# Kernel optimization log

Measured on AMD Instinct MI355X. Metric: run time of the kernel, lower is better.

## Reference

```python
import jax, jax.numpy as jnp
from jax import lax
import numpy as np

B = 128          # batch size
S = 207          # input spatial size implied by outputSpatialSize=[8,8]
N_PTS = 256000
NEG = -1e30      # -inf stand-in for masked max-pooling
# BNReLU channel counts in execution order: 8 resnet blocks x (bn1, bn2), final resnet BN(32), last BN(64)
SIZES = [8,8,8,8,8,16,16,16,16,24,24,24,24,32,32,32,32,64]
OFF = np.cumsum([0] + SIZES)

WSHAPES = dict(conv0=(3,3,1,8),
               c1a=(3,3,8,8), c1b=(3,3,8,8), c2a=(3,3,8,8), c2b=(3,3,8,8),
               c3a=(3,3,8,16), c3b=(3,3,16,16), c3r=(3,3,8,16),
               c4a=(3,3,16,16), c4b=(3,3,16,16),
               c5a=(3,3,16,24), c5b=(3,3,24,24), c5r=(3,3,16,24),
               c6a=(3,3,24,24), c6b=(3,3,24,24),
               c7a=(3,3,24,32), c7b=(3,3,32,32), c7r=(3,3,24,32),
               c8a=(3,3,32,32), c8b=(3,3,32,32),
               conv_last=(5,5,32,64))

def _conv(x, w, stride, padding):
    return lax.conv_general_dilated(x, w, (stride, stride), padding,
                                    dimension_numbers=('NHWC', 'HWIO', 'NHWC'))

def _pool_max(x, win, stride, init):
    return lax.reduce_window(x, init, lax.max, (1, win, win, 1), (1, stride, stride, 1), 'VALID')

def _bnrelu(x, m, g, b):
    # eval-mode BN folded to affine, applied on active sites only (inactive stay exactly 0)
    return m * jax.nn.relu(x * g + b)

def _subconv(x, w, m):
    # submanifold conv == dense conv on zero-filled grid, output restricted to active sites
    return _conv(x, w, 1, 'SAME') * m

def _strided(x, w, m, win, stride):
    # scn.Convolution: output site active iff any active input in its receptive field
    m2 = _pool_max(m, win, stride, 0.0)
    return _conv(x, w, stride, 'VALID') * m2, m2

def _block(x, m, g1, b1, w1, g2, b2, w2, wres, stride):
    # pre-activation basic block from scn.SparseResNet
    h = _bnrelu(x, m, g1, b1)
    if stride == 1:
        h, m2 = _subconv(h, w1, m), m
    else:
        h, m2 = _strided(h, w1, m, 3, 2)
    h = _subconv(_bnrelu(h, m2, g2, b2), w2, m2)
    r = x if wres is None else _strided(x, wres, m, 3, 2)[0]
    return h + r, m2

def _forward(locations, batch_idx, features, bn_gamma, bn_beta, W):
    idx = (batch_idx, locations[:, 0], locations[:, 1], jnp.zeros_like(batch_idx))
    x = jnp.zeros((B, S, S, 1), jnp.float32).at[idx].add(features[:, 0])  # InputLayer (sum dups)
    m = jnp.zeros((B, S, S, 1), jnp.float32).at[idx].set(1.0)             # active-site mask
    g = [bn_gamma[OFF[i]:OFF[i+1]] for i in range(len(SIZES))]
    b = [bn_beta[OFF[i]:OFF[i+1]] for i in range(len(SIZES))]
    x = _subconv(x, W['conv0'], m)                              # 1->8 @ 207x207
    # MaxPooling(pool 3, stride 2) over active sites only
    m2 = _pool_max(m, 3, 2, 0.0)
    x = jnp.where(m2 > 0, _pool_max(jnp.where(m > 0, x, NEG), 3, 2, NEG), 0.0)
    m = m2                                                      # @ 103x103
    blocks = [('c1a', 'c1b', None, 1), ('c2a', 'c2b', None, 1),
              ('c3a', 'c3b', 'c3r', 2), ('c4a', 'c4b', None, 1),
              ('c5a', 'c5b', 'c5r', 2), ('c6a', 'c6b', None, 1),
              ('c7a', 'c7b', 'c7r', 2), ('c8a', 'c8b', None, 1)]
    for i, (k1, k2, kr, st) in enumerate(blocks):
        x, m = _block(x, m, g[2*i], b[2*i], W[k1], g[2*i+1], b[2*i+1], W[k2],
                      None if kr is None else W[kr], st)        # 103->51->25->12
    x = _bnrelu(x, m, g[16], b[16])                             # final resnet BNReLU(32)
    x, m = _strided(x, W['conv_last'], m, 5, 1)                 # 32->64, 12x12 -> 8x8
    x = _bnrelu(x, m, g[17], b[17])
    flat = x.transpose(0, 3, 1, 2).reshape(B, -1)               # SparseToDense + flatten (NCHW order)
    return (flat @ W['w_lin'].T).reshape(B, -1, 1)              # [B, 100, 1]

def setup_inputs():
    key = jax.random.key(0)
    ks = iter(jax.random.split(key, 64))
    inp = {
        'locations': jax.random.randint(next(ks), (N_PTS, 2), 0, S, dtype=jnp.int32),
        'batch_idx': jax.random.randint(next(ks), (N_PTS,), 0, B, dtype=jnp.int32),
        'features': jax.random.normal(next(ks), (N_PTS, 1), jnp.float32),
        'bn_gamma': 1.0 + 0.1 * jax.random.normal(next(ks), (int(OFF[-1]),), jnp.float32),
        'bn_beta': 0.1 * jax.random.normal(next(ks), (int(OFF[-1]),), jnp.float32),
    }
    for name, shp in WSHAPES.items():
        fan_in = int(np.prod(shp[:-1]))
        inp[name] = jax.random.normal(next(ks), shp, jnp.float32) * (2.0 / fan_in) ** 0.5
    inp['w_lin'] = jax.random.normal(next(ks), (100, 64 * 8 * 8), jnp.float32) * (1.0 / 4096.0) ** 0.5
    return inp

def reference(locations, batch_idx, features, bn_gamma, bn_beta, conv0,
              c1a, c1b, c2a, c2b, c3a, c3b, c3r, c4a, c4b, c5a, c5b, c5r,
              c6a, c6b, c7a, c7b, c7r, c8a, c8b, conv_last, w_lin):
    W = dict(conv0=conv0, c1a=c1a, c1b=c1b, c2a=c2a, c2b=c2b, c3a=c3a, c3b=c3b, c3r=c3r,
             c4a=c4a, c4b=c4b, c5a=c5a, c5b=c5b, c5r=c5r, c6a=c6a, c6b=c6b,
             c7a=c7a, c7b=c7b, c7r=c7r, c8a=c8a, c8b=c8b, conv_last=conv_last, w_lin=w_lin)
    return _forward(locations, batch_idx, features, bn_gamma, bn_beta, W)
```

## Files before the change

### kernel.cpp

```cpp
#include <hip/hip_runtime.h>

#define S 207
#define BATCH 128
#define NPTS 256000

static const int OFFS[19] = {0,8,16,24,32,40,56,72,88,104,128,152,176,200,232,264,296,328,392};

__global__ void zero2_kernel(float4* __restrict__ a, float4* __restrict__ b, int n4) {
    int i = blockIdx.x * blockDim.x + threadIdx.x;
    if (i < n4) { a[i] = make_float4(0,0,0,0); b[i] = make_float4(0,0,0,0); }
}

__global__ void zero_kernel(float* __restrict__ p, int n) {
    int i = blockIdx.x * blockDim.x + threadIdx.x;
    if (i < n) p[i] = 0.0f;
}

__global__ void scatter_kernel(const int* __restrict__ loc, const int* __restrict__ bidx,
                               const float* __restrict__ feat,
                               float* __restrict__ xs, float* __restrict__ ms) {
    int t = blockIdx.x * blockDim.x + threadIdx.x;
    if (t >= NPTS) return;
    int b = bidx[t];
    int r = loc[2 * t];
    int c = loc[2 * t + 1];
    int idx = (b * S + r) * S + c;
    atomicAdd(&xs[idx], feat[t]);
    ms[idx] = 1.0f;
}

__global__ __launch_bounds__(256) void conv0_pool_kernel(
    const float* __restrict__ xs, const float* __restrict__ ms,
    const float* __restrict__ w,
    float* __restrict__ x1, float* __restrict__ m1) {
    const int Hout = 103;
    int opix = blockIdx.x * 256 + threadIdx.x;
    int total = BATCH * Hout * Hout;
    if (opix >= total) return;
    int wo = opix % Hout;
    int t = opix / Hout;
    int ho = t % Hout;
    int b  = t / Hout;

    float mv[3][3];
    float mwin = 0.0f;
    #pragma unroll
    for (int pi = 0; pi < 3; ++pi)
        #pragma unroll
        for (int pj = 0; pj < 3; ++pj) {
            float m = ms[(b * S + 2 * ho + pi) * S + 2 * wo + pj];
            mv[pi][pj] = m;
            mwin = fmaxf(mwin, m);
        }
    float* xp = x1 + (size_t)opix * 8;
    if (mwin <= 0.0f) {
        *(float4*)xp = make_float4(0,0,0,0);
        *(float4*)(xp + 4) = make_float4(0,0,0,0);
        m1[opix] = 0.0f;
        return;
    }
    float p[5][5];
    #pragma unroll
    for (int r = 0; r < 5; ++r) {
        int ii = 2 * ho - 1 + r;
        #pragma unroll
        for (int c = 0; c < 5; ++c) {
            int jj = 2 * wo - 1 + c;
            bool ok = ((unsigned)ii < (unsigned)S) && ((unsigned)jj < (unsigned)S);
            p[r][c] = ok ? xs[(b * S + ii) * S + jj] : 0.0f;
        }
    }
    float best[8];
    #pragma unroll
    for (int co = 0; co < 8; ++co) best[co] = -1e30f;
    #pragma unroll
    for (int pi = 0; pi < 3; ++pi)
        #pragma unroll
        for (int pj = 0; pj < 3; ++pj) {
            if (mv[pi][pj] > 0.0f) {
                float acc[8];
                #pragma unroll
                for (int co = 0; co < 8; ++co) acc[co] = 0.0f;
                #pragma unroll
                for (int kh = 0; kh < 3; ++kh)
                    #pragma unroll
                    for (int kw = 0; kw < 3; ++kw) {
                        float x = p[pi + kh][pj + kw];
                        #pragma unroll
                        for (int co = 0; co < 8; ++co)
                            acc[co] = fmaf(x, w[(kh * 3 + kw) * 8 + co], acc[co]);
                    }
                #pragma unroll
                for (int co = 0; co < 8; ++co) best[co] = fmaxf(best[co], acc[co]);
            }
        }
    *(float4*)xp = make_float4(best[0], best[1], best[2], best[3]);
    *(float4*)(xp + 4) = make_float4(best[4], best[5], best[6], best[7]);
    m1[opix] = 1.0f;
}

template <int C, int TILE, int NTX>
__global__ __launch_bounds__(256) void resblock_kernel(
    const float* __restrict__ in, const float* __restrict__ mask,
    const float* __restrict__ w1, const float* __restrict__ w2,
    const float* __restrict__ g1, const float* __restrict__ bb1,
    const float* __restrict__ g2, const float* __restrict__ bb2,
    float* __restrict__ out, int H) {
    constexpr int XT = TILE + 4, HT = TILE + 2;
    constexpr int XA = XT * XT, HA = HT * HT;
    __shared__ float xs[C][XA];
    __shared__ float h1[C][HA];
    __shared__ float msh[XA];

    int tid = threadIdx.x;
    int bid = blockIdx.x;
    int b = bid / (NTX * NTX);
    int t = bid % (NTX * NTX);
    int r0 = (t / NTX) * TILE, c0 = (t % NTX) * TILE;

    float gr[C], br[C];
    #pragma unroll
    for (int c = 0; c < C; ++c) { gr[c] = g1[c]; br[c] = bb1[c]; }

    for (int i = tid; i < XA; i += 256) {
        int py = i / XT, px = i % XT;
        int gy = r0 - 2 + py, gx = c0 - 2 + px;
        bool ok = (unsigned)gy < (unsigned)H && (unsigned)gx < (unsigned)H;
        float m = 0.0f;
        if (ok) m = mask[(size_t)(b * H + gy) * H + gx];
        msh[i] = m;
        if (m > 0.0f) {
            const float* ip = in + ((size_t)(b * H + gy) * H + gx) * C;
            #pragma unroll
            for (int c = 0; c < C; ++c)
                xs[c][i] = m * fmaxf(fmaf(ip[c], gr[c], br[c]), 0.0f);
        } else {
            #pragma unroll
            for (int c = 0; c < C; ++c) xs[c][i] = 0.0f;
        }
    }
    #pragma unroll
    for (int c = 0; c < C; ++c) { gr[c] = g2[c]; br[c] = bb2[c]; }
    __syncthreads();

    for (int pos = tid; pos < HA; pos += 256) {
        int py = pos / HT, px = pos % HT;
        float mc = msh[(py + 1) * XT + px + 1];
        float acc[C];
        #pragma unroll
        for (int co = 0; co < C; ++co) acc[co] = 0.0f;
        if (mc > 0.0f) {
            #pragma unroll
            for (int kh = 0; kh < 3; ++kh)
                #pragma unroll
                for (int kw = 0; kw < 3; ++kw) {
                    int pix = (py + kh) * XT + px + kw;
                    const float* wp = w1 + (kh * 3 + kw) * C * C;
                    #pragma unroll
                    for (int ci = 0; ci < C; ++ci) {
                        float xv = xs[ci][pix];
                        #pragma unroll
                        for (int co = 0; co < C; ++co)
                            acc[co] = fmaf(xv, wp[ci * C + co], acc[co]);
                    }
                }
        }
        #pragma unroll
        for (int co = 0; co < C; ++co)
            h1[co][pos] = mc * fmaxf(fmaf(acc[co] * mc, gr[co], br[co]), 0.0f);
    }
    __syncthreads();

    {
        int ty = tid / TILE, tx = tid % TILE;
        int gy = r0 + ty, gx = c0 + tx;
        if (gy < H && gx < H) {
            float mo = msh[(ty + 2) * XT + tx + 2];
            float acc[C];
            #pragma unroll
            for (int co = 0; co < C; ++co) acc[co] = 0.0f;
            if (mo > 0.0f) {
                #pragma unroll
                for (int kh = 0; kh < 3; ++kh)
                    #pragma unroll
                    for (int kw = 0; kw < 3; ++kw) {
                        int pix = (ty + kh) * HT + tx + kw;
                        const float* wp = w2 + (kh * 3 + kw) * C * C;
                        #pragma unroll
                        for (int ci = 0; ci < C; ++ci) {
                            float xv = h1[ci][pix];
                            #pragma unroll
                            for (int co = 0; co < C; ++co)
                                acc[co] = fmaf(xv, wp[ci * C + co], acc[co]);
                        }
                    }
            }
            const float* rp = in + ((size_t)(b * H + gy) * H + gx) * C;
            float* op = out + ((size_t)(b * H + gy) * H + gx) * C;
            #pragma unroll
            for (int j = 0; j < C; j += 4) {
                float4 r4 = *(const float4*)(rp + j);
                float4 o4;
                o4.x = fmaf(acc[j],     mo, r4.x);
                o4.y = fmaf(acc[j + 1], mo, r4.y);
                o4.z = fmaf(acc[j + 2], mo, r4.z);
                o4.w = fmaf(acc[j + 3], mo, r4.w);
                *(float4*)(op + j) = o4;
            }
        }
    }
}

template <int K, int CIN, int COUT, int COT, bool BN, bool RES>
__global__ __launch_bounds__(256) void fconv_kernel(
    const float* __restrict__ in, const float* __restrict__ w,
    const float* __restrict__ g, const float* __restrict__ bbn,
    const float* __restrict__ mIn, const float* __restrict__ mOut,
    const float* __restrict__ res, float* __restrict__ out,
    int Hin, int Hout, int stride, int pad) {
    const int Win = Hin, Wout = Hout;
    int npix = BATCH * Hout * Wout;
    int opix = blockIdx.x * 256 + threadIdx.x;
    if (opix >= npix) return;
    int co0 = blockIdx.y * COT;
    int wo = opix % Wout;
    int t = opix / Wout;
    int ho = t % Hout;
    int b  = t / Hout;

    float mo = mOut[opix];
    float* op = out + (size_t)opix * COUT + co0;
    if (mo <= 0.0f) {
        #pragma unroll
        for (int j = 0; j < COT; j += 4) {
            float4 r4 = RES ? *(const float4*)(res + (size_t)opix * COUT + co0 + j)
                            : make_float4(0,0,0,0);
            *(float4*)(op + j) = r4;
        }
        return;
    }
    float acc[COT];
    #pragma unroll
    for (int j = 0; j < COT; ++j) acc[j] = 0.0f;

    #pragma unroll
    for (int kh = 0; kh < K; ++kh) {
        int ih = ho * stride + kh - pad;
        if ((unsigned)ih >= (unsigned)Hin) continue;
        #pragma unroll
        for (int kw = 0; kw < K; ++kw) {
            int iw = wo * stride + kw - pad;
            if ((unsigned)iw >= (unsigned)Win) continue;
            int ipix = (b * Hin + ih) * Win + iw;
            float mi = 1.0f;
            if (BN) { mi = mIn[ipix]; if (mi <= 0.0f) continue; }
            const float* ip = in + (size_t)ipix * CIN;
            const float* wp = w + (kh * K + kw) * CIN * COUT + co0;
            #pragma unroll
            for (int ci = 0; ci < CIN; ci += 4) {
                float4 xv = *(const float4*)(ip + ci);
                if (BN) {
                    xv.x = mi * fmaxf(fmaf(xv.x, g[ci],     bbn[ci]),     0.0f);
                    xv.y = mi * fmaxf(fmaf(xv.y, g[ci + 1], bbn[ci + 1]), 0.0f);
                    xv.z = mi * fmaxf(fmaf(xv.z, g[ci + 2], bbn[ci + 2]), 0.0f);
                    xv.w = mi * fmaxf(fmaf(xv.w, g[ci + 3], bbn[ci + 3]), 0.0f);
                }
                #pragma unroll
                for (int j = 0; j < COT; ++j) {
                    acc[j] = fmaf(xv.x, wp[(ci    ) * COUT + j], acc[j]);
                    acc[j] = fmaf(xv.y, wp[(ci + 1) * COUT + j], acc[j]);
                    acc[j] = fmaf(xv.z, wp[(ci + 2) * COUT + j], acc[j]);
                    acc[j] = fmaf(xv.w, wp[(ci + 3) * COUT + j], acc[j]);
                }
            }
        }
    }
    #pragma unroll
    for (int j = 0; j < COT; j += 4) {
        float4 o4;
        o4.x = acc[j] * mo; o4.y = acc[j+1] * mo; o4.z = acc[j+2] * mo; o4.w = acc[j+3] * mo;
        if (RES) {
            float4 r4 = *(const float4*)(res + (size_t)opix * COUT + co0 + j);
            o4.x += r4.x; o4.y += r4.y; o4.z += r4.z; o4.w += r4.w;
        }
        *(float4*)(op + j) = o4;
    }
}

template <int CIN, int COUT, int COT>
__global__ __launch_bounds__(256) void strided_ra_kernel(
    const float* __restrict__ in,
    const float* __restrict__ wR, const float* __restrict__ wA,
    const float* __restrict__ g, const float* __restrict__ bbn,
    const float* __restrict__ mIn, float* __restrict__ mOutBuf,
    float* __restrict__ outR, float* __restrict__ outA,
    int Hin, int Hout) {
    constexpr int NG = COUT / COT;
    int npix = BATCH * Hout * Hout;
    int opix = blockIdx.x * 256 + threadIdx.x;
    if (opix >= npix) return;
    int path = blockIdx.y / NG;
    int co0  = (blockIdx.y % NG) * COT;
    int wo = opix % Hout;
    int t = opix / Hout;
    int ho = t % Hout;
    int b  = t / Hout;

    const float* wsel = path ? wA : wR;
    float acc[COT];
    #pragma unroll
    for (int j = 0; j < COT; ++j) acc[j] = 0.0f;
    float m2 = 0.0f;

    #pragma unroll
    for (int kh = 0; kh < 3; ++kh) {
        int ih = 2 * ho + kh;
        #pragma unroll
        for (int kw = 0; kw < 3; ++kw) {
            int iw = 2 * wo + kw;
            int ipix = (b * Hin + ih) * Hin + iw;
            float mi = mIn[ipix];
            if (mi <= 0.0f) continue;
            m2 = fmaxf(m2, mi);
            const float* ip = in + (size_t)ipix * CIN;
            const float* wp = wsel + (kh * 3 + kw) * CIN * COUT + co0;
            #pragma unroll
            for (int ci = 0; ci < CIN; ci += 4) {
                float4 xv = *(const float4*)(ip + ci);
                if (path) {
                    xv.x = mi * fmaxf(fmaf(xv.x, g[ci],     bbn[ci]),     0.0f);
                    xv.y = mi * fmaxf(fmaf(xv.y, g[ci + 1], bbn[ci + 1]), 0.0f);
                    xv.z = mi * fmaxf(fmaf(xv.z, g[ci + 2], bbn[ci + 2]), 0.0f);
                    xv.w = mi * fmaxf(fmaf(xv.w, g[ci + 3], bbn[ci + 3]), 0.0f);
                }
                #pragma unroll
                for (int j = 0; j < COT; ++j) {
                    acc[j] = fmaf(xv.x, wp[(ci    ) * COUT + j], acc[j]);
                    acc[j] = fmaf(xv.y, wp[(ci + 1) * COUT + j], acc[j]);
                    acc[j] = fmaf(xv.z, wp[(ci + 2) * COUT + j], acc[j]);
                    acc[j] = fmaf(xv.w, wp[(ci + 3) * COUT + j], acc[j]);
                }
            }
        }
    }
    if (blockIdx.y == 0) mOutBuf[opix] = m2;
    float* op = (path ? outA : outR) + (size_t)opix * COUT + co0;
    #pragma unroll
    for (int j = 0; j < COT; j += 4) {
        float4 o4;
        o4.x = acc[j] * m2; o4.y = acc[j+1] * m2; o4.z = acc[j+2] * m2; o4.w = acc[j+3] * m2;
        *(float4*)(op + j) = o4;
    }
}

__global__ void pool_kernel(const float* __restrict__ in, float* __restrict__ out,
                            int Hin, int Win, int Hout, int Wout, int win, int stride) {
    int tid = blockIdx.x * blockDim.x + threadIdx.x;
    int total = BATCH * Hout * Wout;
    if (tid >= total) return;
    int wo = tid % Wout;
    int p = tid / Wout;
    int ho = p % Hout;
    int b  = p / Hout;
    float mx = 0.0f;
    for (int i = 0; i < win; ++i)
        for (int j = 0; j < win; ++j)
            mx = fmaxf(mx, in[(b * Hin + ho * stride + i) * Win + wo * stride + j]);
    out[tid] = mx;
}

__global__ __launch_bounds__(256) void bn_tr_kernel(
    const float* __restrict__ x, const float* __restrict__ m,
    const float* __restrict__ g, const float* __restrict__ bb,
    float* __restrict__ xt) {
    int tid = blockIdx.x * 256 + threadIdx.x;
    if (tid >= BATCH * 4096) return;
    int c = tid & 63, hw = (tid >> 6) & 63, b = tid >> 12;
    float v = m[b * 64 + hw] * fmaxf(fmaf(x[tid], g[c], bb[c]), 0.0f);
    xt[((size_t)b << 12) + c * 64 + hw] = v;
}

__global__ __launch_bounds__(256) void linear_gemm_kernel(
    const float* __restrict__ xt, const float* __restrict__ wl,
    float* __restrict__ out) {
    int o = blockIdx.x;
    int half = threadIdx.x >> 7;
    int b = threadIdx.x & 127;
    int k0 = blockIdx.y * 512 + half * 256;
    const float* xp = xt + ((size_t)b << 12) + k0;
    const float* wp = wl + o * 4096 + k0;
    float acc = 0.0f;
    #pragma unroll 16
    for (int k = 0; k < 256; k += 4) {
        float4 xv = *(const float4*)(xp + k);
        float4 wv = *(const float4*)(wp + k);
        acc = fmaf(xv.x, wv.x, acc); acc = fmaf(xv.y, wv.y, acc);
        acc = fmaf(xv.z, wv.z, acc); acc = fmaf(xv.w, wv.w, acc);
    }
    atomicAdd(&out[b * 100 + o], acc);
}

template <int K, int CIN, int COUT, int COT, bool BN, bool RES>
static inline void fconv(hipStream_t s, const float* in, const float* w,
                         const float* g, const float* bbn,
                         const float* mIn, const float* mOut, const float* res,
                         float* out, int Hin, int Hout, int stride, int pad) {
    int npix = BATCH * Hout * Hout;
    dim3 grid((npix + 255) / 256, COUT / COT);
    fconv_kernel<K, CIN, COUT, COT, BN, RES><<<grid, 256, 0, s>>>(
        in, w, g, bbn, mIn, mOut, res, out, Hin, Hout, stride, pad);
}

template <int CIN, int COUT, int COT>
static inline void strided_ra(hipStream_t s, const float* in, const float* wR, const float* wA,
                              const float* g, const float* bbn, const float* mIn,
                              float* mOutBuf, float* outR, float* outA, int Hin, int Hout) {
    int npix = BATCH * Hout * Hout;
    dim3 grid((npix + 255) / 256, 2 * (COUT / COT));
    strided_ra_kernel<CIN, COUT, COT><<<grid, 256, 0, s>>>(
        in, wR, wA, g, bbn, mIn, mOutBuf, outR, outA, Hin, Hout);
}

extern "C" void kernel_launch(void* const* d_in, const int* in_sizes, int n_in,
                              void* d_out, int out_size, void* d_ws, size_t ws_size,
                              hipStream_t stream) {
    const int*   loc   = (const int*)d_in[0];
    const int*   bidx  = (const int*)d_in[1];
    const float* feat  = (const float*)d_in[2];
    const float* gamma = (const float*)d_in[3];
    const float* beta  = (const float*)d_in[4];
    const float* Wconv0 = (const float*)d_in[5];
    const float* Wc1a = (const float*)d_in[6];
    const float* Wc1b = (const float*)d_in[7];
    const float* Wc2a = (const float*)d_in[8];
    const float* Wc2b = (const float*)d_in[9];
    const float* Wc3a = (const float*)d_in[10];
    const float* Wc3b = (const float*)d_in[11];
    const float* Wc3r = (const float*)d_in[12];
    const float* Wc4a = (const float*)d_in[13];
    const float* Wc4b = (const float*)d_in[14];
    const float* Wc5a = (const float*)d_in[15];
    const float* Wc5b = (const float*)d_in[16];
    const float* Wc5r = (const float*)d_in[17];
    const float* Wc6a = (const float*)d_in[18];
    const float* Wc6b = (const float*)d_in[19];
    const float* Wc7a = (const float*)d_in[20];
    const float* Wc7b = (const float*)d_in[21];
    const float* Wc7r = (const float*)d_in[22];
    const float* Wc8a = (const float*)d_in[23];
    const float* Wc8b = (const float*)d_in[24];
    const float* Wlast = (const float*)d_in[25];
    const float* wlin  = (const float*)d_in[26];

    const size_t SZB = (size_t)BATCH * 103 * 103 * 8;
    const size_t SZM = (size_t)BATCH * 103 * 103;
    float* b0 = (float*)d_ws;
    float* b1 = b0 + SZB;
    float* b2 = b1 + SZB;
    float* m0 = b2 + SZB;
    float* m1 = m0 + SZM;

    const float* G[18];
    const float* Bt[18];
    for (int i = 0; i < 18; ++i) { G[i] = gamma + OFFS[i]; Bt[i] = beta + OFFS[i]; }

    {
        int n = BATCH * S * S;
        zero2_kernel<<<(n / 4 + 255) / 256, 256, 0, stream>>>((float4*)b1, (float4*)b2, n / 4);
        scatter_kernel<<<(NPTS + 255) / 256, 256, 0, stream>>>(loc, bidx, feat, b1, b2);
        int total = BATCH * 103 * 103;
        conv0_pool_kernel<<<(total + 255) / 256, 256, 0, stream>>>(b1, b2, Wconv0, b0, m0);
    }

    resblock_kernel<8, 16, 7><<<dim3(7 * 7 * BATCH), 256, 0, stream>>>(
        b0, m0, Wc1a, Wc1b, G[0], Bt[0], G[1], Bt[1], b1, 103);
    resblock_kernel<8, 16, 7><<<dim3(7 * 7 * BATCH), 256, 0, stream>>>(
        b1, m0, Wc2a, Wc2b, G[2], Bt[2], G[3], Bt[3], b2, 103);
    strided_ra<8, 16, 16>(stream, b2, Wc3r, Wc3a, G[4], Bt[4], m0, m1, b0, b1, 103, 51);
    fconv<3, 16, 16, 8, true, true >(stream, b1, Wc3b, G[5], Bt[5], m1, m1, b0, b2, 51, 51, 1, 1);
    fconv<3, 16, 16, 8, true, false>(stream, b2, Wc4a, G[6], Bt[6], m1, m1, nullptr, b0, 51, 51, 1, 1);
    fconv<3, 16, 16, 8, true, true >(stream, b0, Wc4b, G[7], Bt[7], m1, m1, b2,      b1, 51, 51, 1, 1);
    strided_ra<16, 24, 24>(stream, b1, Wc5r, Wc5a, G[8], Bt[8], m1, m0, b0, b2, 51, 25);
    fconv<3, 24, 24, 8, true, true >(stream, b2, Wc5b, G[9], Bt[9], m0, m0, b0, b1, 25, 25, 1, 1);
    fconv<3, 24, 24, 8, true, false>(stream, b1, Wc6a, G[10], Bt[10], m0, m0, nullptr, b0, 25, 25, 1, 1);
    fconv<3, 24, 24, 8, true, true >(stream, b0, Wc6b, G[11], Bt[11], m0, m0, b1,      b2, 25, 25, 1, 1);
    strided_ra<24, 32, 8>(stream, b2, Wc7r, Wc7a, G[12], Bt[12], m0, m1, b0, b1, 25, 12);
    fconv<3, 32, 32, 4, true, true >(stream, b1, Wc7b, G[13], Bt[13], m1, m1, b0, b2, 12, 12, 1, 1);
    fconv<3, 32, 32, 4, true, false>(stream, b2, Wc8a, G[14], Bt[14], m1, m1, nullptr, b0, 12, 12, 1, 1);
    fconv<3, 32, 32, 4, true, true >(stream, b0, Wc8b, G[15], Bt[15], m1, m1, b2,      b1, 12, 12, 1, 1);
    pool_kernel<<<(BATCH * 64 + 255) / 256, 256, 0, stream>>>(m1, m0, 12, 12, 8, 8, 5, 1);
    fconv<5, 32, 64, 4, true, false>(stream, b1, Wlast, G[16], Bt[16], m1, m0, nullptr, b0, 12, 8, 1, 0);
    bn_tr_kernel<<<(BATCH * 4096 + 255) / 256, 256, 0, stream>>>(b0, m0, G[17], Bt[17], b2);
    zero_kernel<<<(BATCH * 100 + 255) / 256, 256, 0, stream>>>((float*)d_out, BATCH * 100);
    linear_gemm_kernel<<<dim3(100, 8), 256, 0, stream>>>(b2, wlin, (float*)d_out);
}
```

Before: 802.0 us.

## Add tiled downsample kernel, fuse block 4 into resblock, split conv_last over kernel rows

After: 961.3 us. 1.2x slower.

```diff
diff --git a/kernel.cpp b/kernel.cpp
--- a/kernel.cpp
+++ b/kernel.cpp
@@ -11,9 +11,11 @@
     if (i < n4) { a[i] = make_float4(0,0,0,0); b[i] = make_float4(0,0,0,0); }
 }
 
-__global__ void zero_kernel(float* __restrict__ p, int n) {
+__global__ void zero_pair_kernel(float4* __restrict__ a, int n4a,
+                                 float4* __restrict__ b, int n4b) {
     int i = blockIdx.x * blockDim.x + threadIdx.x;
-    if (i < n) p[i] = 0.0f;
+    if (i < n4a) a[i] = make_float4(0,0,0,0);
+    if (i < n4b) b[i] = make_float4(0,0,0,0);
 }
 
 __global__ void scatter_kernel(const int* __restrict__ loc, const int* __restrict__ bidx,
@@ -208,6 +210,85 @@
                 *(float4*)(op + j) = o4;
             }
         }
+    }
+}
+
+template <int CIN, int COUT, int TILE, int NTX>
+__global__ __launch_bounds__(256) void ds_tile_kernel(
+    const float* __restrict__ in,
+    const float* __restrict__ wR, const float* __restrict__ wA,
+    const float* __restrict__ g, const float* __restrict__ bbn,
+    const float* __restrict__ mIn, float* __restrict__ mOut,
+    float* __restrict__ outR, float* __restrict__ outA,
+    int Hin, int Hout) {
+    constexpr int IT = 2 * TILE + 1;
+    constexpr int IA = IT * IT;
+    __shared__ float xs[CIN][IA];
+    __shared__ float msh[IA];
+    int tid = threadIdx.x;
+    int bid = blockIdx.x;
+    int b = bid / (NTX * NTX);
+    int t = bid % (NTX * NTX);
+    int r0 = (t / NTX) * TILE, c0 = (t % NTX) * TILE;
+    int gy0 = 2 * r0, gx0 = 2 * c0;
+
+    for (int i = tid; i < IA; i += 256) {
+        int gy = gy0 + i / IT, gx = gx0 + i % IT;
+        float m = 0.0f;
+        if (gy < Hin && gx < Hin) m = mIn[(size_t)(b * Hin + gy) * Hin + gx];
+        msh[i] = m;
+        if (m > 0.0f) {
+            const float* ip = in + ((size_t)(b * Hin + gy) * Hin + gx) * CIN;
+            #pragma unroll
+            for (int c = 0; c < CIN; c += 4) {
+                float4 v = *(const float4*)(ip + c);
+                xs[c][i] = v.x; xs[c + 1][i] = v.y; xs[c + 2][i] = v.z; xs[c + 3][i] = v.w;
+            }
+        } else {
+            #pragma unroll
+            for (int c = 0; c < CIN; ++c) xs[c][i] = 0.0f;
+        }
+    }
+    __syncthreads();
+
+    int oy = tid / TILE, ox = tid % TILE;
+    int ho = r0 + oy, wo = c0 + ox;
+    if (ho >= Hout || wo >= Hout) return;
+    float accR[COUT], accA[COUT];
+    #pragma unroll
+    for (int j = 0; j < COUT; ++j) { accR[j] = 0.0f; accA[j] = 0.0f; }
+    float m2 = 0.0f;
+    #pragma unroll
+    for (int kh = 0; kh < 3; ++kh)
+        #pragma unroll
+        for (int kw = 0; kw < 3; ++kw) {
+            int pix = (2 * oy + kh) * IT + 2 * ox + kw;
+            float mi = msh[pix];
+            if (mi <= 0.0f) continue;
+            m2 = fmaxf(m2, mi);
+            const float* wpR = wR + (kh * 3 + kw) * CIN * COUT;
+            const float* wpA = wA + (kh * 3 + kw) * CIN * COUT;
+            #pragma unroll
+            for (int ci = 0; ci < CIN; ++ci) {
+                float xv = xs[ci][pix];
+                float hv = mi * fmaxf(fmaf(xv, g[ci], bbn[ci]), 0.0f);
+                #pragma unroll
+                for (int j = 0; j < COUT; ++j) {
+                    accR[j] = fmaf(xv, wpR[ci * COUT + j], accR[j]);
+                    accA[j] = fmaf(hv, wpA[ci * COUT + j], accA[j]);
+                }
+            }
+        }
+    int opix = (b * Hout + ho) * Hout + wo;
+    mOut[opix] = m2;
+    float* opR = outR + (size_t)opix * COUT;
+    float* opA = outA + (size_t)opix * COUT;
+    #pragma unroll
+    for (int j = 0; j < COUT; j += 4) {
+        float4 r4 = make_float4(accR[j] * m2, accR[j+1] * m2, accR[j+2] * m2, accR[j+3] * m2);
+        float4 a4 = make_float4(accA[j] * m2, accA[j+1] * m2, accA[j+2] * m2, accA[j+3] * m2);
+        *(float4*)(opR + j) = r4;
+        *(float4*)(opA + j) = a4;
     }
 }
 
@@ -351,6 +432,54 @@
         o4.x = acc[j] * m2; o4.y = acc[j+1] * m2; o4.z = acc[j+2] * m2; o4.w = acc[j+3] * m2;
         *(float4*)(op + j) = o4;
     }
+}
+
+__global__ __launch_bounds__(256) void conv_last_kernel(
+    const float* __restrict__ in, const float* __restrict__ w,
+    const float* __restrict__ g, const float* __restrict__ bbn,
+    const float* __restrict__ mIn, const float* __restrict__ mOut,
+    float* __restrict__ out) {
+    constexpr int COT = 8;
+    int opix = blockIdx.x * 256 + threadIdx.x;
+    int co0 = blockIdx.y * COT;
+    int kh = blockIdx.z;
+    int wo = opix & 7;
+    int t = opix >> 3;
+    int ho = t & 7;
+    int b  = t >> 3;
+    float mo = mOut[opix];
+    if (mo <= 0.0f) return;
+    int ih = ho + kh;
+    float acc[COT];
+    #pragma unroll
+    for (int j = 0; j < COT; ++j) acc[j] = 0.0f;
+    #pragma unroll
+    for (int kw = 0; kw < 5; ++kw) {
+        int iw = wo + kw;
+        int ipix = (b * 12 + ih) * 12 + iw;
+        float mi = mIn[ipix];
+        if (mi <= 0.0f) continue;
+        const float* ip = in + (size_t)ipix * 32;
+        const float* wp = w + (kh * 5 + kw) * 32 * 64 + co0;
+        #pragma unroll
+        for (int ci = 0; ci < 32; ci += 4) {
+            float4 xv = *(const float4*)(ip + ci);
+            xv.x = mi * fmaxf(fmaf(xv.x, g[ci],     bbn[ci]),     0.0f);
+            xv.y = mi * fmaxf(fmaf(xv.y, g[ci + 1], bbn[ci + 1]), 0.0f);
+            xv.z = mi * fmaxf(fmaf(xv.z, g[ci + 2], bbn[ci + 2]), 0.0f);
+            xv.w = mi * fmaxf(fmaf(xv.w, g[ci + 3], bbn[ci + 3]), 0.0f);
+            #pragma unroll
+            for (int j = 0; j < COT; ++j) {
+                acc[j] = fmaf(xv.x, wp[(ci    ) * 64 + j], acc[j]);
+                acc[j] = fmaf(xv.y, wp[(ci + 1) * 64 + j], acc[j]);
+                acc[j] = fmaf(xv.z, wp[(ci + 2) * 64 + j], acc[j]);
+                acc[j] = fmaf(xv.w, wp[(ci + 3) * 64 + j], acc[j]);
+            }
+        }
+    }
+    float* op = out + (size_t)opix * 64 + co0;
+    #pragma unroll
+    for (int j = 0; j < COT; ++j) atomicAdd(op + j, acc[j] * mo);
 }
 
 __global__ void pool_kernel(const float* __restrict__ in, float* __restrict__ out,
@@ -476,10 +605,11 @@
         b0, m0, Wc1a, Wc1b, G[0], Bt[0], G[1], Bt[1], b1, 103);
     resblock_kernel<8, 16, 7><<<dim3(7 * 7 * BATCH), 256, 0, stream>>>(
         b1, m0, Wc2a, Wc2b, G[2], Bt[2], G[3], Bt[3], b2, 103);
-    strided_ra<8, 16, 16>(stream, b2, Wc3r, Wc3a, G[4], Bt[4], m0, m1, b0, b1, 103, 51);
+    ds_tile_kernel<8, 16, 16, 4><<<dim3(4 * 4 * BATCH), 256, 0, stream>>>(
+        b2, Wc3r, Wc3a, G[4], Bt[4], m0, m1, b0, b1, 103, 51);
     fconv<3, 16, 16, 8, true, true >(stream, b1, Wc3b, G[5], Bt[5], m1, m1, b0, b2, 51, 51, 1, 1);
-    fconv<3, 16, 16, 8, true, false>(stream, b2, Wc4a, G[6], Bt[6], m1, m1, nullptr, b0, 51, 51, 1, 1);
-    fconv<3, 16, 16, 8, true, true >(stream, b0, Wc4b, G[7], Bt[7], m1, m1, b2,      b1, 51, 51, 1, 1);
+    resblock_kernel<16, 16, 4><<<dim3(4 * 4 * BATCH), 256, 0, stream>>>(
+        b2, m1, Wc4a, Wc4b, G[6], Bt[6], G[7], Bt[7], b1, 51);
     strided_ra<16, 24, 24>(stream, b1, Wc5r, Wc5a, G[8], Bt[8], m1, m0, b0, b2, 51, 25);
     fconv<3, 24, 24, 8, true, true >(stream, b2, Wc5b, G[9], Bt[9], m0, m0, b0, b1, 25, 25, 1, 1);
     fconv<3, 24, 24, 8, true, false>(stream, b1, Wc6a, G[10], Bt[10], m0, m0, nullptr, b0, 25, 25, 1, 1);
@@ -488,9 +618,11 @@
     fconv<3, 32, 32, 4, true, true >(stream, b1, Wc7b, G[13], Bt[13], m1, m1, b0, b2, 12, 12, 1, 1);
     fconv<3, 32, 32, 4, true, false>(stream, b2, Wc8a, G[14], Bt[14], m1, m1, nullptr, b0, 12, 12, 1, 1);
     fconv<3, 32, 32, 4, true, true >(stream, b0, Wc8b, G[15], Bt[15], m1, m1, b2,      b1, 12, 12, 1, 1);
+    zero_pair_kernel<<<(BATCH * 8 * 8 * 64 / 4 + 255) / 256, 256, 0, stream>>>(
+        (float4*)b0, BATCH * 8 * 8 * 64 / 4, (float4*)d_out, BATCH * 100 / 4);
     pool_kernel<<<(BATCH * 64 + 255) / 256, 256, 0, stream>>>(m1, m0, 12, 12, 8, 8, 5, 1);
-    fconv<5, 32, 64, 4, true, false>(stream, b1, Wlast, G[16], Bt[16], m1, m0, nullptr, b0, 12, 8, 1, 0);
+    conv_last_kernel<<<dim3(BATCH * 64 / 256, 8, 5), 256, 0, stream>>>(
+        b1, Wlast, G[16], Bt[16], m1, m0, b0);
     bn_tr_kernel<<<(BATCH * 4096 + 255) / 256, 256, 0, stream>>>(b0, m0, G[17], Bt[17], b2);
-    zero_kernel<<<(BATCH * 100 + 255) / 256, 256, 0, stream>>>((float*)d_out, BATCH * 100);
     linear_gemm_kernel<<<dim3(100, 8), 256, 0, stream>>>(b2, wlin, (float*)d_out);
 }
```
